# Kernel optimization log

Hardware: AMD Instinct MI355X
Metric: run time of the kernel (lower is better)

## Reference

```python
import jax, jax.numpy as jnp
import numpy as np

BATCH, FIELD0, EMB = 1024, 32, 64
LAYER_SIZES = (128, 128, 128)  # split_half=True -> hidden field sizes [32, 64, 64]


def setup_inputs() -> dict:
    key = jax.random.key(0)
    ks = jax.random.split(key, 7)
    x = jax.random.normal(ks[0], (BATCH, FIELD0, EMB), dtype=jnp.float32)
    # Conv1D(kernel_size=1) weights: (in_channels=f0*fi, filters=layer_size), plus bias.
    field_sizes = [FIELD0]
    params = {}
    for i, size in enumerate(LAYER_SIZES):
        fi = field_sizes[-1]
        fan_in = FIELD0 * fi
        scale = 1.0 / np.sqrt(fan_in)
        params[f"W{i}"] = jax.random.normal(ks[1 + 2 * i], (fan_in, size), dtype=jnp.float32) * scale
        params[f"b{i}"] = jnp.zeros((size,), dtype=jnp.float32)
        field_sizes.append(size // 2 if i != len(LAYER_SIZES) - 1 else size)
    return {"x": x, **params}


def reference(x, W0, b0, W1, b1, W2, b2):
    # CIN: outer product + 1x1 conv (a matmul over the flattened field-pair axis)
    # fused as a single bilinear contraction per layer:
    #   cur[b,k,e] = sum_{i,j} x[b,i,e] * hidden[b,j,e] * W[i,j,k] + b[k]
    Ws = [(W0, b0), (W1, b1), (W2, b2)]
    f0 = x.shape[1]
    hidden = x
    final_outputs = []
    n_layers = len(Ws)
    for idx, (W, b) in enumerate(Ws):
        fi = hidden.shape[1]
        Wr = W.reshape(f0, fi, W.shape[-1])  # channel m = i*fi + j (row-major reshape)
        cur = jnp.einsum('bie,bje,ijk->bke', x, hidden, Wr) + b[None, :, None]
        # activation=None -> linear
        if idx != n_layers - 1:
            half = cur.shape[1] // 2
            hidden, direct = cur[:, :half, :], cur[:, half:, :]
        else:
            direct = cur
        final_outputs.append(direct)
    result = jnp.concatenate(final_outputs, axis=1)  # (B, 64+64+128, E)
    return jnp.sum(result, axis=-1)  # (B, 256)
```

## Files before the change

### kernel.cpp

```cpp
#include <hip/hip_runtime.h>
#include <cstdint>


typedef _Float16 half8  __attribute__((ext_vector_type(8)));
typedef _Float16 half4_ __attribute__((ext_vector_type(4)));
typedef _Float16 half2_ __attribute__((ext_vector_type(2)));
typedef float    f32x4  __attribute__((ext_vector_type(4)));

__global__ void pack_w_all(const float* __restrict__ W0, _Float16* __restrict__ Wt0,
                           const float* __restrict__ W1, _Float16* __restrict__ Wt1,
                           const float* __restrict__ W2, _Float16* __restrict__ Wt2)
{
    __shared__ _Float16 ldsT[128 * 33];
    const int blk = blockIdx.x, t = threadIdx.x;
    const float* W;
    _Float16* Wt;
    int c;
    if (blk < 32)       { W = W0; Wt = Wt0; c = blk; }
    else if (blk < 96)  { W = W1; Wt = Wt1; c = blk - 32; }
    else                { W = W2; Wt = Wt2; c = blk - 96; }

    for (int p = t; p < 32 * 128; p += 256) {
        int kk = p >> 7, m = p & 127;
        ldsT[m * 33 + kk] = (_Float16)W[(size_t)(c * 32 + kk) * 128 + m];
    }
    __syncthreads();
    int m = t >> 1, kk0 = (t & 1) * 16;
    half8 v0, v1;
#pragma unroll
    for (int i = 0; i < 8; ++i) {
        v0[i] = ldsT[m * 33 + kk0 + i];
        v1[i] = ldsT[m * 33 + kk0 + 8 + i];
    }
    *(half8*)(Wt + (size_t)c * 4096 + t * 16)     = v0;
    *(half8*)(Wt + (size_t)c * 4096 + t * 16 + 8) = v1;
}

template<int NCH, int ISH, int PH>
__device__ __forceinline__ void kloop_t(f32x4 (&acc)[4][4],
    const _Float16* __restrict__ WtL, const _Float16* __restrict__ hb,
    const _Float16* __restrict__ sX, int lr, int q, int w)
{
#pragma unroll
    for (int mt = 0; mt < 4; ++mt)
#pragma unroll
        for (int nt = 0; nt < 4; ++nt)
            acc[mt][nt] = f32x4{0.0f, 0.0f, 0.0f, 0.0f};

    constexpr int HC = NCH / 4;
    const int c0 = w * HC;
    const _Float16* aG = WtL + (size_t)c0 * 4096 + lr * 32 + q * 8;
    const _Float16* hP = hb + lr * PH + q * 8;
    const _Float16* xP = sX + lr;

    half8 afA[4], afB[4], hvA[4], hvB[4];
    _Float16 xsA[4], xsB[4];

    auto pf = [&](half8* af, half8* hv, _Float16* xs, int cc) {
        const int c  = c0 + cc;
        const int i  = c >> ISH;
        const int j0 = (c & ((1 << ISH) - 1)) << 5;
        const _Float16* ag = aG + (size_t)cc * 4096;
#pragma unroll
        for (int mt = 0; mt < 4; ++mt)
            af[mt] = *(const half8*)(ag + mt * 512);
        const _Float16* hh = hP + j0;
        const _Float16* xb = xP + (i << 6);
#pragma unroll
        for (int nt = 0; nt < 4; ++nt) {
            hv[nt] = *(const half8*)(hh + nt * (PH * 16));
            xs[nt] = xb[nt * 16];
        }
    };
    auto cp = [&](half8* af, half8* hv, _Float16* xs) {
#pragma unroll
        for (int nt = 0; nt < 4; ++nt) {
            half2_ xv2 = {xs[nt], xs[nt]};
            half8 xv8 = __builtin_shufflevector(xv2, xv2, 0, 1, 0, 1, 0, 1, 0, 1);
            half8 bf = hv[nt] * xv8;
#pragma unroll
            for (int mt = 0; mt < 4; ++mt)
                acc[mt][nt] = __builtin_amdgcn_mfma_f32_16x16x32_f16(
                    af[mt], bf, acc[mt][nt], 0, 0, 0);
        }
    };

    pf(afA, hvA, xsA, 0);
    for (int cc = 0; cc < HC; cc += 2) {
        pf(afB, hvB, xsB, cc + 1);
        cp(afA, hvA, xsA);
        if (cc + 2 < HC) pf(afA, hvA, xsA, cc + 2);
        cp(afB, hvB, xsB);
    }
}

__global__ __launch_bounds__(256, 2)
void cin_fused(const float* __restrict__ x,
               const _Float16* __restrict__ Wt0,
               const _Float16* __restrict__ Wt1,
               const float* __restrict__ bs0,
               const float* __restrict__ bs1,
               _Float16* __restrict__ S0,
               _Float16* __restrict__ S1,
               _Float16* __restrict__ S2)
{
    __shared__ alignas(16) char smem[47104];
    _Float16* sX   = (_Float16*)smem;
    _Float16* R_A  = (_Float16*)(smem + 4096);
    _Float16* R_B  = (_Float16*)(smem + 13312);
    _Float16* XC16 = (_Float16*)(smem + 22528);

    const int t = threadIdx.x, lane = t & 63, w = t >> 6;
    const int lr = lane & 15, q = lane >> 4;
    const int b = blockIdx.x;

    {
        const float4* xv = (const float4*)(x + (size_t)b * 2048);
#pragma unroll
        for (int s = 0; s < 2; ++s) {
            int p4 = t + s * 256;
            float4 v = xv[p4];
            int idx = p4 * 4, i = idx >> 6, e0 = idx & 63;
            _Float16 h0 = (_Float16)v.x, h1 = (_Float16)v.y;
            _Float16 h2 = (_Float16)v.z, h3 = (_Float16)v.w;
            half4_ pk = {h0, h1, h2, h3};
            *(half4_*)(sX + i * 64 + e0) = pk;
            *(half4_*)(R_B + i * 72 + e0) = pk;
            R_A[(e0 + 0) * 40 + i] = h0;
            R_A[(e0 + 1) * 40 + i] = h1;
            R_A[(e0 + 2) * 40 + i] = h2;
            R_A[(e0 + 3) * 40 + i] = h3;
        }
    }
    __syncthreads();

    const int it = w & 1;
    const half8 aF0 = *(const half8*)(R_B + (it * 16 + lr) * 72 + q * 8);
    const half8 aF1 = *(const half8*)(R_B + (it * 16 + lr) * 72 + q * 8 + 32);

    f32x4 acc[4][4];

    auto xchg_write = [&]() {
#pragma unroll
        for (int mt = 0; mt < 4; ++mt) {
            if (mt == w) continue;
            const int slot = mt * 3 + (w > mt ? w - 1 : w);
#pragma unroll
            for (int cc = 0; cc < 2; ++cc) {
                half8 hv8;
#pragma unroll
                for (int r = 0; r < 4; ++r) {
                    hv8[r]     = (_Float16)acc[mt][cc * 2][r];
                    hv8[4 + r] = (_Float16)acc[mt][cc * 2 + 1][r];
                }
                *(half8*)(XC16 + slot * 1024 + cc * 512 + lane * 8) = hv8;
            }
        }
    };

    auto finish = [&](f32x4 (&aw)[4], const float* bs,
                      _Float16* hJ, _Float16* hT, bool wantT) {
#pragma unroll
        for (int p = 0; p < 3; ++p) {
#pragma unroll
            for (int cc = 0; cc < 2; ++cc) {
                half8 hv8 = *(const half8*)(XC16 + (w * 3 + p) * 1024
                                            + cc * 512 + lane * 8);
#pragma unroll
                for (int r = 0; r < 4; ++r) {
                    aw[cc * 2][r]     += (float)hv8[r];
                    aw[cc * 2 + 1][r] += (float)hv8[4 + r];
                }
            }
        }
        const int jb = w * 16 + q * 4;
        const float b0f = bs[jb + 0], b1f = bs[jb + 1];
        const float b2f = bs[jb + 2], b3f = bs[jb + 3];
#pragma unroll
        for (int nt = 0; nt < 4; ++nt) {
            const int e = nt * 16 + lr;
            half4_ vh;
            vh[0] = (_Float16)(aw[nt][0] + b0f);
            vh[1] = (_Float16)(aw[nt][1] + b1f);
            vh[2] = (_Float16)(aw[nt][2] + b2f);
            vh[3] = (_Float16)(aw[nt][3] + b3f);
            hJ[(jb + 0) * 72 + e] = vh[0];
            hJ[(jb + 1) * 72 + e] = vh[1];
            hJ[(jb + 2) * 72 + e] = vh[2];
            hJ[(jb + 3) * 72 + e] = vh[3];
            if (wantT) *(half4_*)(hT + e * 72 + jb) = vh;
        }
    };
    auto combine_epi = [&](const float* bs, _Float16* hJ, _Float16* hT,
                           bool wantT) {
        if (w == 0)      finish(acc[0], bs, hJ, hT, wantT);
        else if (w == 1) finish(acc[1], bs, hJ, hT, wantT);
        else if (w == 2) finish(acc[2], bs, hJ, hT, wantT);
        else             finish(acc[3], bs, hJ, hT, wantT);
    };

    auto sgemm = [&](const _Float16* hJ, int fi, _Float16* Sdst) {
        const int nT = fi >> 3;
        for (int tt = w; tt < nT; tt += 4) {
            const int jt = tt >> 1;
            f32x4 sa = {0.0f, 0.0f, 0.0f, 0.0f};
            half8 bv0 = *(const half8*)(hJ + (jt * 16 + lr) * 72 + q * 8);
            half8 bv1 = *(const half8*)(hJ + (jt * 16 + lr) * 72 + q * 8 + 32);
            sa = __builtin_amdgcn_mfma_f32_16x16x32_f16(aF0, bv0, sa, 0, 0, 0);
            sa = __builtin_amdgcn_mfma_f32_16x16x32_f16(aF1, bv1, sa, 0, 0, 0);
#pragma unroll
            for (int r = 0; r < 4; ++r)
                Sdst[(size_t)b * (32 * fi) + (it * 16 + q * 4 + r) * fi
                     + jt * 16 + lr] = (_Float16)sa[r];
        }
    };

    sgemm(R_B, 32, S0);
    kloop_t<32, 0, 40>(acc, Wt0, R_A, sX, lr, q, w);
    xchg_write();
    __syncthreads();
    combine_epi(bs0, R_A, R_B, true);
    __syncthreads();
    sgemm(R_A, 64, S1);
    kloop_t<64, 1, 72>(acc, Wt1, R_B, sX, lr, q, w);
    xchg_write();
    __syncthreads();
    combine_epi(bs1, R_A, nullptr, false);
    __syncthreads();
    sgemm(R_A, 64, S2);
}

__global__ __launch_bounds__(256, 4)
void cin_direct(const _Float16* __restrict__ S0v, const _Float16* __restrict__ S1v,
                const _Float16* __restrict__ S2v,
                const _Float16* __restrict__ Wt0, const _Float16* __restrict__ Wt1,
                const _Float16* __restrict__ Wt2,
                const float* __restrict__ bs0, const float* __restrict__ bs1,
                const float* __restrict__ bs2,
                float* __restrict__ out)
{
    __shared__ f32x4 red[3][64];
    const int t = threadIdx.x, lane = t & 63, kh = t >> 6;
    const int lr = lane & 15, q = lane >> 4;
    const int task = blockIdx.x;

    const _Float16 *S, *Wt;
    const float* bias;
    int fan, nch, dm0, ob, idx;
    if (task < 256)      { S = S0v; Wt = Wt0; bias = bs0; fan = 1024; nch = 32; dm0 = 64; ob = 0;   idx = task; }
    else if (task < 512) { S = S1v; Wt = Wt1; bias = bs1; fan = 2048; nch = 64; dm0 = 64; ob = 64;  idx = task - 256; }
    else                 { S = S2v; Wt = Wt2; bias = bs2; fan = 2048; nch = 64; dm0 = 0;  ob = 128; idx = task - 512; }
    const int bt = idx & 63, kt = idx >> 6;
    const int bbase = bt * 16;
    const int hq = nch >> 2, c0 = kh * hq;

    const _Float16* aG = Wt + (size_t)(dm0 + kt * 16 + lr) * 32 + q * 8
                            + (size_t)c0 * 4096;
    const _Float16* bG = S + (size_t)(bbase + lr) * fan + q * 8 + c0 * 32;

    f32x4 acc = {0.0f, 0.0f, 0.0f, 0.0f};
    half8 aA = *(const half8*)(aG);
    half8 bA = *(const half8*)(bG);
    for (int c = 0; c < hq; c += 2) {
        half8 aB = *(const half8*)(aG + (size_t)(c + 1) * 4096);
        half8 bB = *(const half8*)(bG + (c + 1) * 32);
        acc = __builtin_amdgcn_mfma_f32_16x16x32_f16(aA, bA, acc, 0, 0, 0);
        if (c + 2 < hq) {
            aA = *(const half8*)(aG + (size_t)(c + 2) * 4096);
            bA = *(const half8*)(bG + (c + 2) * 32);
        }
        acc = __builtin_amdgcn_mfma_f32_16x16x32_f16(aB, bB, acc, 0, 0, 0);
    }
    if (kh != 0) red[kh - 1][lane] = acc;
    __syncthreads();
    if (kh == 0) {
#pragma unroll
        for (int p = 0; p < 3; ++p) {
            f32x4 o = red[p][lane];
#pragma unroll
            for (int r = 0; r < 4; ++r) acc[r] += o[r];
        }
#pragma unroll
        for (int r = 0; r < 4; ++r) {
            int kl = kt * 16 + q * 4 + r;
            out[(size_t)(bbase + lr) * 256 + ob + kl]
                = acc[r] + 64.0f * bias[dm0 + kl];
        }
    }
}

extern "C" void kernel_launch(void* const* d_in, const int* in_sizes, int n_in,
                              void* d_out, int out_size, void* d_ws, size_t ws_size,
                              hipStream_t stream)
{
    const float* x  = (const float*)d_in[0];
    const float* W0 = (const float*)d_in[1];
    const float* b0 = (const float*)d_in[2];
    const float* W1 = (const float*)d_in[3];
    const float* b1 = (const float*)d_in[4];
    const float* W2 = (const float*)d_in[5];
    const float* b2 = (const float*)d_in[6];
    float* out = (float*)d_out;

    char* ws = (char*)d_ws;
    _Float16* Wt0 = (_Float16*)(ws + 0);
    _Float16* Wt1 = (_Float16*)(ws + 262144);
    _Float16* Wt2 = (_Float16*)(ws + 786432);
    _Float16* S0  = (_Float16*)(ws + 1310720);
    _Float16* S1  = (_Float16*)(ws + 3407872);
    _Float16* S2  = (_Float16*)(ws + 7602176);
    (void)in_sizes; (void)n_in; (void)out_size; (void)ws_size;

    hipLaunchKernelGGL(pack_w_all, dim3(160), dim3(256), 0, stream,
                       W0, Wt0, W1, Wt1, W2, Wt2);

    hipLaunchKernelGGL(cin_fused, dim3(1024), dim3(256), 0, stream,
                       x, Wt0, Wt1, b0, b1, S0, S1, S2);

    hipLaunchKernelGGL(cin_direct, dim3(1024), dim3(256), 0, stream,
                       S0, S1, S2, Wt0, Wt1, Wt2, b0, b1, b2, out);
}
```

Before: 115.5 us.

## Halve cross-wave exchange buffer in two rounds, raise occupancy, prioritize MFMA

The cross-wave reduction of split-K accumulators now runs in two rounds, each reducing two of the four output tiles. This halves the LDS exchange buffer from 12 slots to 6, shrinking shared memory to 34816 bytes, and launch bounds go up to 4 blocks per CU for higher occupancy. The MFMA loop also raises wave priority with s_setprio. The trade-off is two extra block barriers per layer, idle waves during each reduction half, and tighter register limits that may cause spills.

```diff
diff --git a/kernel.cpp b/kernel.cpp
--- a/kernel.cpp
+++ b/kernel.cpp
@@ -73,6 +73,7 @@
         }
     };
     auto cp = [&](half8* af, half8* hv, _Float16* xs) {
+        __builtin_amdgcn_s_setprio(1);
 #pragma unroll
         for (int nt = 0; nt < 4; ++nt) {
             half2_ xv2 = {xs[nt], xs[nt]};
@@ -83,6 +84,7 @@
                 acc[mt][nt] = __builtin_amdgcn_mfma_f32_16x16x32_f16(
                     af[mt], bf, acc[mt][nt], 0, 0, 0);
         }
+        __builtin_amdgcn_s_setprio(0);
     };
 
     pf(afA, hvA, xsA, 0);
@@ -94,7 +96,7 @@
     }
 }
 
-__global__ __launch_bounds__(256, 2)
+__global__ __launch_bounds__(256, 4)
 void cin_fused(const float* __restrict__ x,
                const _Float16* __restrict__ Wt0,
                const _Float16* __restrict__ Wt1,
@@ -104,7 +106,7 @@
                _Float16* __restrict__ S1,
                _Float16* __restrict__ S2)
 {
-    __shared__ alignas(16) char smem[47104];
+    __shared__ alignas(16) char smem[34816];
     _Float16* sX   = (_Float16*)smem;
     _Float16* R_A  = (_Float16*)(smem + 4096);
     _Float16* R_B  = (_Float16*)(smem + 13312);
@@ -140,39 +142,36 @@
 
     f32x4 acc[4][4];
 
-    auto xchg_write = [&]() {
-#pragma unroll
-        for (int mt = 0; mt < 4; ++mt) {
-            if (mt == w) continue;
-            const int slot = mt * 3 + (w > mt ? w - 1 : w);
+    auto xw_pair = [&](const f32x4 (&a)[4], int slot) {
+#pragma unroll
+        for (int cc = 0; cc < 2; ++cc) {
+            half8 hv8;
+#pragma unroll
+            for (int r = 0; r < 4; ++r) {
+                hv8[r]     = (_Float16)a[cc * 2][r];
+                hv8[4 + r] = (_Float16)a[cc * 2 + 1][r];
+            }
+            *(half8*)(XC16 + slot * 1024 + cc * 512 + lane * 8) = hv8;
+        }
+    };
+    auto xr_sum = [&](f32x4 (&a)[4], int tgt) {
+#pragma unroll
+        for (int p = 0; p < 3; ++p) {
 #pragma unroll
             for (int cc = 0; cc < 2; ++cc) {
-                half8 hv8;
+                half8 hv8 = *(const half8*)(XC16 + (tgt * 3 + p) * 1024
+                                            + cc * 512 + lane * 8);
 #pragma unroll
                 for (int r = 0; r < 4; ++r) {
-                    hv8[r]     = (_Float16)acc[mt][cc * 2][r];
-                    hv8[4 + r] = (_Float16)acc[mt][cc * 2 + 1][r];
-                }
-                *(half8*)(XC16 + slot * 1024 + cc * 512 + lane * 8) = hv8;
-            }
-        }
-    };
-
-    auto finish = [&](f32x4 (&aw)[4], const float* bs,
-                      _Float16* hJ, _Float16* hT, bool wantT) {
-#pragma unroll
-        for (int p = 0; p < 3; ++p) {
-#pragma unroll
-            for (int cc = 0; cc < 2; ++cc) {
-                half8 hv8 = *(const half8*)(XC16 + (w * 3 + p) * 1024
-                                            + cc * 512 + lane * 8);
-#pragma unroll
-                for (int r = 0; r < 4; ++r) {
-                    aw[cc * 2][r]     += (float)hv8[r];
-                    aw[cc * 2 + 1][r] += (float)hv8[4 + r];
+                    a[cc * 2][r]     += (float)hv8[r];
+                    a[cc * 2 + 1][r] += (float)hv8[4 + r];
                 }
             }
         }
+    };
+
+    auto epi_rows = [&](const f32x4 (&a)[4], const float* bs,
+                        _Float16* hJ, _Float16* hT, bool wantT) {
         const int jb = w * 16 + q * 4;
         const float b0f = bs[jb + 0], b1f = bs[jb + 1];
         const float b2f = bs[jb + 2], b3f = bs[jb + 3];
@@ -180,10 +179,10 @@
         for (int nt = 0; nt < 4; ++nt) {
             const int e = nt * 16 + lr;
             half4_ vh;
-            vh[0] = (_Float16)(aw[nt][0] + b0f);
-            vh[1] = (_Float16)(aw[nt][1] + b1f);
-            vh[2] = (_Float16)(aw[nt][2] + b2f);
-            vh[3] = (_Float16)(aw[nt][3] + b3f);
+            vh[0] = (_Float16)(a[nt][0] + b0f);
+            vh[1] = (_Float16)(a[nt][1] + b1f);
+            vh[2] = (_Float16)(a[nt][2] + b2f);
+            vh[3] = (_Float16)(a[nt][3] + b3f);
             hJ[(jb + 0) * 72 + e] = vh[0];
             hJ[(jb + 1) * 72 + e] = vh[1];
             hJ[(jb + 2) * 72 + e] = vh[2];
@@ -191,12 +190,24 @@
             if (wantT) *(half4_*)(hT + e * 72 + jb) = vh;
         }
     };
+
     auto combine_epi = [&](const float* bs, _Float16* hJ, _Float16* hT,
                            bool wantT) {
-        if (w == 0)      finish(acc[0], bs, hJ, hT, wantT);
-        else if (w == 1) finish(acc[1], bs, hJ, hT, wantT);
-        else if (w == 2) finish(acc[2], bs, hJ, hT, wantT);
-        else             finish(acc[3], bs, hJ, hT, wantT);
+        if (w == 0)      { xw_pair(acc[1], 3); }
+        else if (w == 1) { xw_pair(acc[0], 0); }
+        else if (w == 2) { xw_pair(acc[0], 1); xw_pair(acc[1], 4); }
+        else             { xw_pair(acc[0], 2); xw_pair(acc[1], 5); }
+        __syncthreads();
+        if (w == 0)      { xr_sum(acc[0], 0); epi_rows(acc[0], bs, hJ, hT, wantT); }
+        else if (w == 1) { xr_sum(acc[1], 1); epi_rows(acc[1], bs, hJ, hT, wantT); }
+        __syncthreads();
+        if (w == 0)      { xw_pair(acc[2], 0); xw_pair(acc[3], 3); }
+        else if (w == 1) { xw_pair(acc[2], 1); xw_pair(acc[3], 4); }
+        else if (w == 2) { xw_pair(acc[3], 5); }
+        else             { xw_pair(acc[2], 2); }
+        __syncthreads();
+        if (w == 2)      { xr_sum(acc[2], 0); epi_rows(acc[2], bs, hJ, hT, wantT); }
+        else if (w == 3) { xr_sum(acc[3], 1); epi_rows(acc[3], bs, hJ, hT, wantT); }
     };
 
     auto sgemm = [&](const _Float16* hJ, int fi, _Float16* Sdst) {
@@ -217,14 +228,10 @@
 
     sgemm(R_B, 32, S0);
     kloop_t<32, 0, 40>(acc, Wt0, R_A, sX, lr, q, w);
-    xchg_write();
-    __syncthreads();
     combine_epi(bs0, R_A, R_B, true);
     __syncthreads();
     sgemm(R_A, 64, S1);
     kloop_t<64, 1, 72>(acc, Wt1, R_B, sX, lr, q, w);
-    xchg_write();
-    __syncthreads();
     combine_epi(bs1, R_A, nullptr, false);
     __syncthreads();
     sgemm(R_A, 64, S2);
```

New measurement: 246.1 us. +113.1%, slower.
